# Performance work log

Hardware: AMD Instinct MI355X
Metric: run time of the kernel (lower is better)

The kernel has to match this reference:

```python
import jax, jax.numpy as jnp
import numpy as np

TEMPERATURE = 1.0
WEIGHT = 1.0


def _transitivity_sum(rel):
    """rel: [N, N] relation probabilities for one (batch, relation) slice.
    Computes sum_{a,b,c} relu(rel[a,b] - rel[a,c] * rel[b,c]) via a scan over c
    (outer product of column c), keeping memory at O(N^2) instead of O(N^3)."""
    def step(acc, col):  # col = rel[:, c], shape [N]
        viol = jax.nn.relu(rel - col[:, None] * col[None, :])  # [N, N]
        return acc + jnp.sum(viol), None
    acc, _ = jax.lax.scan(step, jnp.zeros((), rel.dtype), rel.T)
    return acc


def setup_inputs() -> dict:
    key = jax.random.key(0)
    B, N, R = 2, 512, 4
    relation_logits = jax.random.normal(key, (B, N, N, R), dtype=jnp.float32)
    entity_masks = jnp.ones((B, N), dtype=jnp.int32)
    return {"relation_logits": relation_logits, "entity_masks": entity_masks}


def reference(relation_logits, entity_masks):
    B, N, _, R = relation_logits.shape
    probs = jax.nn.sigmoid(relation_logits / TEMPERATURE)  # [B, N, N, R]
    m = (entity_masks > 0).astype(probs.dtype)             # [B, N]
    rel = probs * m[:, :, None, None] * m[:, None, :, None]
    # flatten (batch, relation) and vmap the per-matrix cubic reduction
    rel_br = jnp.transpose(rel, (0, 3, 1, 2)).reshape(B * R, N, N)
    per = jax.vmap(_transitivity_sum)(rel_br)              # [B*R]
    # per-batch loss = sum_r / R; final = weight * mean over batch
    return WEIGHT * jnp.sum(per) / (R * B)
```

## Files before the change

kernel.cpp:

```cpp
#include <hip/hip_runtime.h>
#include <math.h>

#define N      512
#define RNUM   4
#define BNUM   2
#define NSLICE (RNUM * BNUM)
#define TILE   128
#define CT     32
#define LSTR   136
#define CSPLIT 16
#define NCOLB  16
#define SCALE  0.0625f

typedef _Float16 half2_t __attribute__((ext_vector_type(2)));

__device__ __forceinline__ unsigned int h2u(half2_t h) {
  return __builtin_bit_cast(unsigned int, h);
}
__device__ __forceinline__ half2_t u2h(unsigned int u) {
  return __builtin_bit_cast(half2_t, u);
}

#if __has_builtin(__builtin_amdgcn_fdot2)
__device__ __forceinline__ float fdot2_(half2_t a, half2_t b, float c) {
  return __builtin_amdgcn_fdot2(a, b, c, false);
}
#else
__device__ __forceinline__ float fdot2_(half2_t a, half2_t b, float c) {
  return c + (float)a.x * (float)b.x + (float)a.y * (float)b.y;
}
#endif

__device__ __forceinline__ unsigned pk_fnma_bl(unsigned a, unsigned b, unsigned c) {
  unsigned d;
  asm("v_pk_fma_f16 %0, %1, %2, %3 op_sel:[0,0,0] op_sel_hi:[0,1,1] neg_lo:[1,0,0] neg_hi:[1,0,0]"
      : "=v"(d) : "v"(a), "v"(b), "v"(c));
  return d;
}
__device__ __forceinline__ unsigned pk_fnma_bh(unsigned a, unsigned b, unsigned c) {
  unsigned d;
  asm("v_pk_fma_f16 %0, %1, %2, %3 op_sel:[1,0,0] op_sel_hi:[1,1,1] neg_lo:[1,0,0] neg_hi:[1,0,0]"
      : "=v"(d) : "v"(a), "v"(b), "v"(c));
  return d;
}

__device__ __forceinline__ float sigmoidf_(float x) {
  return 1.0f / (1.0f + __expf(-x));
}

__device__ __forceinline__ unsigned packh2(float a, float b) {
  half2_t h = {(_Float16)a, (_Float16)b};
  return h2u(h);
}

__global__ void zero_out_kernel(float* out) { out[0] = 0.0f; }

__global__ __launch_bounds__(256) void prep_f16_kernel(const float* __restrict__ logits,
                                                       const int* __restrict__ masks,
                                                       _Float16* __restrict__ P,
                                                       float* __restrict__ out) {
  if (blockIdx.x == 0 && threadIdx.x == 0) out[0] = 0.0f;
  int t = blockIdx.x * 256 + threadIdx.x;
  int b = t >> 16;
  int rem4 = t & (N * N / 4 - 1);
  int i = rem4 >> 7;
  int j4 = rem4 & 127;
  const float4* Lp = ((const float4*)logits) + ((size_t)(b * N + i) * N + 4 * j4);
  float4 l0 = Lp[0], l1 = Lp[1], l2 = Lp[2], l3 = Lp[3];
  int4 mj = *(const int4*)(masks + b * N + 4 * j4);
  float mi = (masks[b * N + i] > 0) ? 1.0f : 0.0f;
  float m0 = mi * ((mj.x > 0) ? 1.0f : 0.0f);
  float m1 = mi * ((mj.y > 0) ? 1.0f : 0.0f);
  float m2 = mi * ((mj.z > 0) ? 1.0f : 0.0f);
  float m3 = mi * ((mj.w > 0) ? 1.0f : 0.0f);
  size_t off = (size_t)i * N + 4 * j4;
  _Float16* Pb = P + (size_t)b * RNUM * N * N + off;
  {
    uint2 v = {packh2(m0 * sigmoidf_(l0.x), m1 * sigmoidf_(l1.x)),
               packh2(m2 * sigmoidf_(l2.x), m3 * sigmoidf_(l3.x))};
    *(uint2*)(Pb + 0 * (size_t)N * N) = v;
  }
  {
    uint2 v = {packh2(m0 * sigmoidf_(l0.y), m1 * sigmoidf_(l1.y)),
               packh2(m2 * sigmoidf_(l2.y), m3 * sigmoidf_(l3.y))};
    *(uint2*)(Pb + 1 * (size_t)N * N) = v;
  }
  {
    uint2 v = {packh2(m0 * sigmoidf_(l0.z), m1 * sigmoidf_(l1.z)),
               packh2(m2 * sigmoidf_(l2.z), m3 * sigmoidf_(l3.z))};
    *(uint2*)(Pb + 2 * (size_t)N * N) = v;
  }
  {
    uint2 v = {packh2(m0 * sigmoidf_(l0.w), m1 * sigmoidf_(l1.w)),
               packh2(m2 * sigmoidf_(l2.w), m3 * sigmoidf_(l3.w))};
    *(uint2*)(Pb + 3 * (size_t)N * N) = v;
  }
}

__global__ __launch_bounds__(256, 4) void work_f16_kernel(const _Float16* __restrict__ P,
                                                          float* __restrict__ out) {
  __shared__ __align__(16) _Float16 tA[CT][LSTR];
  __shared__ __align__(16) _Float16 tB[CT][LSTR];
  __shared__ float wsum[4];

  const int tid = threadIdx.x;
  const int bid = blockIdx.x;

  if (bid < NCOLB) {
    const int s    = bid >> 1;
    const int half = bid & 1;
    const int c    = half * 256 + tid;
    const _Float16* col = P + (size_t)s * N * N + c;
    float sum = 0.0f;
#pragma unroll 16
    for (int a = 0; a < N; ++a) sum += (float)col[(size_t)a * N];
    float v = sum * ((float)N - sum);
    for (int off = 32; off > 0; off >>= 1) v += __shfl_down(v, off, 64);
    const int wid = tid >> 6;
    if ((tid & 63) == 0) wsum[wid] = v;
    __syncthreads();
    if (tid == 0)
      atomicAdd(out, (wsum[0] + wsum[1] + wsum[2] + wsum[3]) * SCALE);
    return;
  }

  const int m  = bid - NCOLB;
  const int bt = m & 3;
  const int at = (m >> 2) & 3;
  const int s  = (m >> 4) & 7;
  const int cz = m >> 7;
  const int a0 = at * TILE;
  const int b0 = bt * TILE;
  const int c0 = cz * CT;

  const int ta = tid & 15;
  const int tb = tid >> 4;

  const _Float16* Ph = P + (size_t)s * N * N;

  {
    const int u   = tid & 127;
    const int h   = tid >> 7;
    const int isB = u >> 6;
    const int p   = u & 63;
    const int r0  = (isB ? b0 : a0) + 2 * p;
    const int cc0 = c0 + h * 16;
    const _Float16* s0row = Ph + (size_t)r0 * N + cc0;
    const _Float16* s1row = s0row + N;
    _Float16* dst = isB ? &tB[h * 16][2 * p] : &tA[h * 16][2 * p];
    uint4 q0 = ((const uint4*)s0row)[0];
    uint4 q1 = ((const uint4*)s0row)[1];
    uint4 r0v = ((const uint4*)s1row)[0];
    uint4 r1v = ((const uint4*)s1row)[1];
    unsigned int w0[8] = {q0.x, q0.y, q0.z, q0.w, q1.x, q1.y, q1.z, q1.w};
    unsigned int w1[8] = {r0v.x, r0v.y, r0v.z, r0v.w, r1v.x, r1v.y, r1v.z, r1v.w};
#pragma unroll
    for (int k = 0; k < 8; ++k) {
      unsigned int lo = (w1[k] << 16) | (w0[k] & 0xFFFFu);
      unsigned int hi = (w1[k] & 0xFFFF0000u) | (w0[k] >> 16);
      *(unsigned int*)(dst + (size_t)(2 * k) * LSTR)     = lo;
      *(unsigned int*)(dst + (size_t)(2 * k + 1) * LSTR) = hi;
    }
  }

  unsigned rabw[8][4];
#pragma unroll
  for (int x = 0; x < 8; ++x) {
    int ga = a0 + ta * 8 + x;
    uint4 q = *(const uint4*)(Ph + (size_t)ga * N + b0 + tb * 8);
    rabw[x][0] = q.x; rabw[x][1] = q.y; rabw[x][2] = q.z; rabw[x][3] = q.w;
  }

  float acc[8];
  unsigned q16[8];
#pragma unroll
  for (int x = 0; x < 8; ++x) { acc[x] = 0.0f; q16[x] = 0u; }

  const half2_t kOne = {(_Float16)1.0f, (_Float16)1.0f};

  __syncthreads();

#pragma unroll 1
  for (int cg = 0; cg < CT / 4; ++cg) {
#pragma unroll
    for (int dc = 0; dc < 4; ++dc) {
      const int c = cg * 4 + dc;
      uint4 ua = *(const uint4*)&tA[c][ta * 8];
      uint4 ub = *(const uint4*)&tB[c][tb * 8];
      unsigned aw[4] = {ua.x, ua.y, ua.z, ua.w};
      unsigned bw[4] = {ub.x, ub.y, ub.z, ub.w};
#pragma unroll
      for (int k = 0; k < 4; ++k) {
#pragma unroll
        for (int yp = 0; yp < 4; ++yp) {
          unsigned tl = pk_fnma_bl(aw[k], bw[yp], rabw[2 * k][yp]);
          q16[2 * k] = h2u(u2h(q16[2 * k]) + u2h(tl & 0x7FFF7FFFu));
          unsigned th = pk_fnma_bh(aw[k], bw[yp], rabw[2 * k + 1][yp]);
          q16[2 * k + 1] = h2u(u2h(q16[2 * k + 1]) + u2h(th & 0x7FFF7FFFu));
        }
      }
    }
#pragma unroll
    for (int x = 0; x < 8; ++x) {
      acc[x] = fdot2_(u2h(q16[x]), kOne, acc[x]);
      q16[x] = 0u;
    }
  }

  float tsum = 0.0f;
#pragma unroll
  for (int x = 0; x < 8; ++x) tsum += acc[x];

  for (int off = 32; off > 0; off >>= 1) tsum += __shfl_down(tsum, off, 64);

  const int wid = tid >> 6;
  if ((tid & 63) == 0) wsum[wid] = tsum;
  __syncthreads();
  if (tid == 0)
    atomicAdd(out, (wsum[0] + wsum[1] + wsum[2] + wsum[3]) * SCALE);
}

#define FCT    64
#define FSTR   132
#define FCSPL  4

__global__ __launch_bounds__(256, 2) void work_f32_fallback(const float* __restrict__ logits,
                                                            const int* __restrict__ masks,
                                                            float* __restrict__ out) {
  __shared__ __align__(16) float tA[FCT][FSTR];
  __shared__ __align__(16) float tB[FCT][FSTR];
  __shared__ float wsum[4];

  const int tid = threadIdx.x;
  const int bid = blockIdx.x;

  if (bid < NCOLB) {
    const int s    = bid >> 1;
    const int half = bid & 1;
    const int c    = half * 256 + tid;
    const int bb   = s >> 2;
    const int r    = s & 3;
    const int* mrow = masks + bb * N;
    float mc = (mrow[c] > 0) ? 1.0f : 0.0f;
    float sum = 0.0f;
#pragma unroll 4
    for (int a = 0; a < N; ++a) {
      float ma = (mrow[a] > 0) ? 1.0f : 0.0f;
      size_t idx = ((size_t)(bb * N + a) * N + c) * RNUM + r;
      sum += sigmoidf_(logits[idx]) * ma * mc;
    }
    float v = sum * ((float)N - sum);
    for (int off = 32; off > 0; off >>= 1) v += __shfl_down(v, off, 64);
    const int wid = tid >> 6;
    if ((tid & 63) == 0) wsum[wid] = v;
    __syncthreads();
    if (tid == 0)
      atomicAdd(out, (wsum[0] + wsum[1] + wsum[2] + wsum[3]) * SCALE);
    return;
  }

  const int m  = bid - NCOLB;
  const int bt = m & 3;
  const int at = (m >> 2) & 3;
  const int s  = (m >> 4) & 7;
  const int cz = m >> 7;
  const int a0 = at * TILE;
  const int b0 = bt * TILE;
  const int bb = s >> 2;
  const int r  = s & 3;
  const int cbeg = cz * (N / FCSPL);
  const int cend = cbeg + (N / FCSPL);

  const int ta = tid & 15;
  const int tb = tid >> 4;
  const int* mrow = masks + bb * N;

  float rab[8][8];
#pragma unroll
  for (int x = 0; x < 8; ++x) {
    int ra = a0 + ((x >> 2) << 6) + ta * 4 + (x & 3);
    float ma = (mrow[ra] > 0) ? 1.0f : 0.0f;
#pragma unroll
    for (int y = 0; y < 8; ++y) {
      int cb = b0 + ((y >> 2) << 6) + tb * 4 + (y & 3);
      float mb = (mrow[cb] > 0) ? 1.0f : 0.0f;
      size_t idx = ((size_t)(bb * N + ra) * N + cb) * RNUM + r;
      rab[x][y] = sigmoidf_(logits[idx]) * ma * mb;
    }
  }

  float acc[8][2];
#pragma unroll
  for (int x = 0; x < 8; ++x) { acc[x][0] = 0.0f; acc[x][1] = 0.0f; }

  for (int c0 = cbeg; c0 < cend; c0 += FCT) {
    __syncthreads();
#pragma unroll
    for (int it = 0; it < 32; ++it) {
      int e = it * 256 + tid;
      int c = e & 63;
      int i = e >> 6;
      int pc = ((((i >> 2) ^ ((c >> 2) & 31)) & 31) << 2) | (i & 3);
      float mc = (mrow[c0 + c] > 0) ? 1.0f : 0.0f;
      {
        float mi = (mrow[a0 + i] > 0) ? 1.0f : 0.0f;
        size_t idx = ((size_t)(bb * N + a0 + i) * N + (c0 + c)) * RNUM + r;
        tA[c][pc] = sigmoidf_(logits[idx]) * mi * mc;
      }
      {
        float mi = (mrow[b0 + i] > 0) ? 1.0f : 0.0f;
        size_t idx = ((size_t)(bb * N + b0 + i) * N + (c0 + c)) * RNUM + r;
        tB[c][pc] = sigmoidf_(logits[idx]) * mi * mc;
      }
    }
    __syncthreads();

#pragma unroll 2
    for (int cg = 0; cg < FCT / 4; ++cg) {
      const float* pa = &tA[cg * 4][((ta ^ cg) & 31) << 2];
      const float* pb = &tB[cg * 4][((tb ^ cg) & 31) << 2];
#pragma unroll
      for (int dc = 0; dc < 4; ++dc) {
        float4 a0v = *(const float4*)(pa + dc * FSTR);
        float4 a1v = *(const float4*)(pa + dc * FSTR + 64);
        float4 b0v = *(const float4*)(pb + dc * FSTR);
        float4 b1v = *(const float4*)(pb + dc * FSTR + 64);
        float avv[8] = {a0v.x, a0v.y, a0v.z, a0v.w, a1v.x, a1v.y, a1v.z, a1v.w};
        float bvv[8] = {b0v.x, b0v.y, b0v.z, b0v.w, b1v.x, b1v.y, b1v.z, b1v.w};
#pragma unroll
        for (int x = 0; x < 8; ++x) {
#pragma unroll
          for (int y = 0; y < 4; ++y)
            acc[x][0] += fabsf(fmaf(-avv[x], bvv[y], rab[x][y]));
#pragma unroll
          for (int y = 4; y < 8; ++y)
            acc[x][1] += fabsf(fmaf(-avv[x], bvv[y], rab[x][y]));
        }
      }
    }
  }

  float tsum = 0.0f;
#pragma unroll
  for (int x = 0; x < 8; ++x) tsum += acc[x][0] + acc[x][1];
  for (int off = 32; off > 0; off >>= 1) tsum += __shfl_down(tsum, off, 64);
  const int wid = tid >> 6;
  if ((tid & 63) == 0) wsum[wid] = tsum;
  __syncthreads();
  if (tid == 0)
    atomicAdd(out, (wsum[0] + wsum[1] + wsum[2] + wsum[3]) * SCALE);
}

extern "C" void kernel_launch(void* const* d_in, const int* in_sizes, int n_in,
                              void* d_out, int out_size, void* d_ws, size_t ws_size,
                              hipStream_t stream) {
  const float* logits = (const float*)d_in[0];
  const int*   masks  = (const int*)d_in[1];
  float*       out    = (float*)d_out;

  const size_t P_BYTES = (size_t)NSLICE * N * N * sizeof(_Float16);

  if (ws_size >= P_BYTES) {
    _Float16* P = (_Float16*)d_ws;
    prep_f16_kernel<<<(BNUM * N * N / 4) / 256, 256, 0, stream>>>(logits, masks, P, out);
    const int nblocks = NCOLB + 4 * 4 * NSLICE * CSPLIT;
    work_f16_kernel<<<nblocks, 256, 0, stream>>>(P, out);
  } else {
    zero_out_kernel<<<1, 1, 0, stream>>>(out);
    const int nblocks = NCOLB + 4 * 4 * NSLICE * FCSPL;
    work_f32_fallback<<<nblocks, 256, 0, stream>>>(logits, masks, out);
  }
}
```

Baseline: 115.2 us.

## Replace packed-f16 inner loop with f32 FMA and abs on 512-thread blocks

The main tile kernel now turns the fp16 staged tiles into fp32 in shared memory and computes |r_ab - r_ac*r_bc| with scalar fp32 fmaf and fabsf. This replaces the packed v_pk_fma_f16 path that used two-level fp16/fp32 accumulation. Blocks grow to 512 threads, with each thread covering 8x4 outputs instead of 8x8, and the column-sum blocks are cut to one per slice. The aim is better precision and more occupancy, at the cost of half the packed arithmetic throughput and twice the shared-memory footprint.

```diff
diff --git a/kernel.cpp b/kernel.cpp
--- a/kernel.cpp
+++ b/kernel.cpp
@@ -7,50 +7,24 @@
 #define NSLICE (RNUM * BNUM)
 #define TILE   128
 #define CT     32
-#define LSTR   136
+#define LSTRF  132
 #define CSPLIT 16
-#define NCOLB  16
+#define NCOLB  8
 #define SCALE  0.0625f
 
 typedef _Float16 half2_t __attribute__((ext_vector_type(2)));
 
-__device__ __forceinline__ unsigned int h2u(half2_t h) {
-  return __builtin_bit_cast(unsigned int, h);
-}
 __device__ __forceinline__ half2_t u2h(unsigned int u) {
   return __builtin_bit_cast(half2_t, u);
 }
 
-#if __has_builtin(__builtin_amdgcn_fdot2)
-__device__ __forceinline__ float fdot2_(half2_t a, half2_t b, float c) {
-  return __builtin_amdgcn_fdot2(a, b, c, false);
-}
-#else
-__device__ __forceinline__ float fdot2_(half2_t a, half2_t b, float c) {
-  return c + (float)a.x * (float)b.x + (float)a.y * (float)b.y;
-}
-#endif
-
-__device__ __forceinline__ unsigned pk_fnma_bl(unsigned a, unsigned b, unsigned c) {
-  unsigned d;
-  asm("v_pk_fma_f16 %0, %1, %2, %3 op_sel:[0,0,0] op_sel_hi:[0,1,1] neg_lo:[1,0,0] neg_hi:[1,0,0]"
-      : "=v"(d) : "v"(a), "v"(b), "v"(c));
-  return d;
-}
-__device__ __forceinline__ unsigned pk_fnma_bh(unsigned a, unsigned b, unsigned c) {
-  unsigned d;
-  asm("v_pk_fma_f16 %0, %1, %2, %3 op_sel:[1,0,0] op_sel_hi:[1,1,1] neg_lo:[1,0,0] neg_hi:[1,0,0]"
-      : "=v"(d) : "v"(a), "v"(b), "v"(c));
-  return d;
-}
-
 __device__ __forceinline__ float sigmoidf_(float x) {
   return 1.0f / (1.0f + __expf(-x));
 }
 
 __device__ __forceinline__ unsigned packh2(float a, float b) {
   half2_t h = {(_Float16)a, (_Float16)b};
-  return h2u(h);
+  return __builtin_bit_cast(unsigned, h);
 }
 
 __global__ void zero_out_kernel(float* out) { out[0] = 0.0f; }
@@ -97,19 +71,18 @@
   }
 }
 
-__global__ __launch_bounds__(256, 4) void work_f16_kernel(const _Float16* __restrict__ P,
+__global__ __launch_bounds__(512, 8) void work_f16_kernel(const _Float16* __restrict__ P,
                                                           float* __restrict__ out) {
-  __shared__ __align__(16) _Float16 tA[CT][LSTR];
-  __shared__ __align__(16) _Float16 tB[CT][LSTR];
-  __shared__ float wsum[4];
+  __shared__ __align__(16) float tA[CT][LSTRF];
+  __shared__ __align__(16) float tB[CT][LSTRF];
+  __shared__ float wsum[8];
 
   const int tid = threadIdx.x;
   const int bid = blockIdx.x;
 
   if (bid < NCOLB) {
-    const int s    = bid >> 1;
-    const int half = bid & 1;
-    const int c    = half * 256 + tid;
+    const int s = bid;
+    const int c = tid;
     const _Float16* col = P + (size_t)s * N * N + c;
     float sum = 0.0f;
 #pragma unroll 16
@@ -119,8 +92,12 @@
     const int wid = tid >> 6;
     if ((tid & 63) == 0) wsum[wid] = v;
     __syncthreads();
-    if (tid == 0)
-      atomicAdd(out, (wsum[0] + wsum[1] + wsum[2] + wsum[3]) * SCALE);
+    if (tid == 0) {
+      float t = 0.0f;
+#pragma unroll
+      for (int w = 0; w < 8; ++w) t += wsum[w];
+      atomicAdd(out, t * SCALE);
+    }
     return;
   }
 
@@ -133,77 +110,63 @@
   const int b0 = bt * TILE;
   const int c0 = cz * CT;
 
-  const int ta = tid & 15;
-  const int tb = tid >> 4;
+  const int ta  = tid & 15;
+  const int tbg = tid >> 5;
+
+  const int tbgq = tid >> 4;
+  (void)tbg;
 
   const _Float16* Ph = P + (size_t)s * N * N;
 
   {
-    const int u   = tid & 127;
-    const int h   = tid >> 7;
-    const int isB = u >> 6;
-    const int p   = u & 63;
-    const int r0  = (isB ? b0 : a0) + 2 * p;
-    const int cc0 = c0 + h * 16;
-    const _Float16* s0row = Ph + (size_t)r0 * N + cc0;
-    const _Float16* s1row = s0row + N;
-    _Float16* dst = isB ? &tB[h * 16][2 * p] : &tA[h * 16][2 * p];
-    uint4 q0 = ((const uint4*)s0row)[0];
-    uint4 q1 = ((const uint4*)s0row)[1];
-    uint4 r0v = ((const uint4*)s1row)[0];
-    uint4 r1v = ((const uint4*)s1row)[1];
-    unsigned int w0[8] = {q0.x, q0.y, q0.z, q0.w, q1.x, q1.y, q1.z, q1.w};
-    unsigned int w1[8] = {r0v.x, r0v.y, r0v.z, r0v.w, r1v.x, r1v.y, r1v.z, r1v.w};
-#pragma unroll
-    for (int k = 0; k < 8; ++k) {
-      unsigned int lo = (w1[k] << 16) | (w0[k] & 0xFFFFu);
-      unsigned int hi = (w1[k] & 0xFFFF0000u) | (w0[k] >> 16);
-      *(unsigned int*)(dst + (size_t)(2 * k) * LSTR)     = lo;
-      *(unsigned int*)(dst + (size_t)(2 * k + 1) * LSTR) = hi;
-    }
-  }
-
-  unsigned rabw[8][4];
+    const int r   = tid & 127;
+    const int oct = tid >> 7;
+    const _Float16* sa = Ph + (size_t)(a0 + r) * N + c0 + oct * 8;
+    const _Float16* sb = Ph + (size_t)(b0 + r) * N + c0 + oct * 8;
+    uint4 qa = *(const uint4*)sa;
+    uint4 qb = *(const uint4*)sb;
+    unsigned wa[4] = {qa.x, qa.y, qa.z, qa.w};
+    unsigned wb[4] = {qb.x, qb.y, qb.z, qb.w};
+#pragma unroll
+    for (int k = 0; k < 4; ++k) {
+      half2_t ha = u2h(wa[k]);
+      half2_t hb = u2h(wb[k]);
+      tA[oct * 8 + 2 * k    ][r] = (float)ha.x;
+      tA[oct * 8 + 2 * k + 1][r] = (float)ha.y;
+      tB[oct * 8 + 2 * k    ][r] = (float)hb.x;
+      tB[oct * 8 + 2 * k + 1][r] = (float)hb.y;
+    }
+  }
+
+  float rabf[8][4];
 #pragma unroll
   for (int x = 0; x < 8; ++x) {
     int ga = a0 + ta * 8 + x;
-    uint4 q = *(const uint4*)(Ph + (size_t)ga * N + b0 + tb * 8);
-    rabw[x][0] = q.x; rabw[x][1] = q.y; rabw[x][2] = q.z; rabw[x][3] = q.w;
+    uint2 q = *(const uint2*)(Ph + (size_t)ga * N + b0 + tbgq * 4);
+    half2_t h0 = u2h(q.x);
+    half2_t h1 = u2h(q.y);
+    rabf[x][0] = (float)h0.x; rabf[x][1] = (float)h0.y;
+    rabf[x][2] = (float)h1.x; rabf[x][3] = (float)h1.y;
   }
 
   float acc[8];
-  unsigned q16[8];
-#pragma unroll
-  for (int x = 0; x < 8; ++x) { acc[x] = 0.0f; q16[x] = 0u; }
-
-  const half2_t kOne = {(_Float16)1.0f, (_Float16)1.0f};
+#pragma unroll
+  for (int x = 0; x < 8; ++x) acc[x] = 0.0f;
 
   __syncthreads();
 
-#pragma unroll 1
-  for (int cg = 0; cg < CT / 4; ++cg) {
-#pragma unroll
-    for (int dc = 0; dc < 4; ++dc) {
-      const int c = cg * 4 + dc;
-      uint4 ua = *(const uint4*)&tA[c][ta * 8];
-      uint4 ub = *(const uint4*)&tB[c][tb * 8];
-      unsigned aw[4] = {ua.x, ua.y, ua.z, ua.w};
-      unsigned bw[4] = {ub.x, ub.y, ub.z, ub.w};
-#pragma unroll
-      for (int k = 0; k < 4; ++k) {
-#pragma unroll
-        for (int yp = 0; yp < 4; ++yp) {
-          unsigned tl = pk_fnma_bl(aw[k], bw[yp], rabw[2 * k][yp]);
-          q16[2 * k] = h2u(u2h(q16[2 * k]) + u2h(tl & 0x7FFF7FFFu));
-          unsigned th = pk_fnma_bh(aw[k], bw[yp], rabw[2 * k + 1][yp]);
-          q16[2 * k + 1] = h2u(u2h(q16[2 * k + 1]) + u2h(th & 0x7FFF7FFFu));
-        }
-      }
-    }
+#pragma unroll 2
+  for (int c = 0; c < CT; ++c) {
+    float4 a0v = *(const float4*)&tA[c][ta * 8];
+    float4 a1v = *(const float4*)&tA[c][ta * 8 + 4];
+    float4 b0v = *(const float4*)&tB[c][tbgq * 4];
+    float av[8] = {a0v.x, a0v.y, a0v.z, a0v.w, a1v.x, a1v.y, a1v.z, a1v.w};
+    float bv[4] = {b0v.x, b0v.y, b0v.z, b0v.w};
 #pragma unroll
     for (int x = 0; x < 8; ++x) {
-      acc[x] = fdot2_(u2h(q16[x]), kOne, acc[x]);
-      q16[x] = 0u;
+#pragma unroll
+      for (int y = 0; y < 4; ++y)
+        acc[x] += fabsf(fmaf(-av[x], bv[y], rabf[x][y]));
     }
   }
 
@@ -216,13 +179,18 @@
   const int wid = tid >> 6;
   if ((tid & 63) == 0) wsum[wid] = tsum;
   __syncthreads();
-  if (tid == 0)
-    atomicAdd(out, (wsum[0] + wsum[1] + wsum[2] + wsum[3]) * SCALE);
+  if (tid == 0) {
+    float t = 0.0f;
+#pragma unroll
+    for (int w = 0; w < 8; ++w) t += wsum[w];
+    atomicAdd(out, t * SCALE);
+  }
 }
 
 #define FCT    64
 #define FSTR   132
 #define FCSPL  4
+#define FNCOLB 16
 
 __global__ __launch_bounds__(256, 2) void work_f32_fallback(const float* __restrict__ logits,
                                                             const int* __restrict__ masks,
@@ -234,7 +202,7 @@
   const int tid = threadIdx.x;
   const int bid = blockIdx.x;
 
-  if (bid < NCOLB) {
+  if (bid < FNCOLB) {
     const int s    = bid >> 1;
     const int half = bid & 1;
     const int c    = half * 256 + tid;
@@ -259,7 +227,7 @@
     return;
   }
 
-  const int m  = bid - NCOLB;
+  const int m  = bid - FNCOLB;
   const int bt = m & 3;
   const int at = (m >> 2) & 3;
   const int s  = (m >> 4) & 7;
@@ -364,10 +332,10 @@
     _Float16* P = (_Float16*)d_ws;
     prep_f16_kernel<<<(BNUM * N * N / 4) / 256, 256, 0, stream>>>(logits, masks, P, out);
     const int nblocks = NCOLB + 4 * 4 * NSLICE * CSPLIT;
-    work_f16_kernel<<<nblocks, 256, 0, stream>>>(P, out);
+    work_f16_kernel<<<nblocks, 512, 0, stream>>>(P, out);
   } else {
     zero_out_kernel<<<1, 1, 0, stream>>>(out);
-    const int nblocks = NCOLB + 4 * 4 * NSLICE * FCSPL;
+    const int nblocks = FNCOLB + 4 * 4 * NSLICE * FCSPL;
     work_f32_fallback<<<nblocks, 256, 0, stream>>>(logits, masks, out);
   }
 }
```

Measured after the change: 127.8 us. 1.11x slower.

## Process two c-chunks per block and accumulate each product via fdot2 into f32

Applied to the files above, without the earlier changes.

Each block now stages two 32-column chunks of the c dimension into two shared buffers, halving the number of c-split blocks. The second chunk's global loads are issued before compute on the first chunk begins. The inner loop drops the inline-asm packed FNMA and the f16 partial accumulator: it computes rab - a*b in half2, takes the absolute value via a sign mask, and adds it straight into f32 with fdot2. This trades the cheaper f16 accumulation for one dot instruction per pair and raises launch_bounds occupancy to 8, which may cause register pressure or spills.

```diff
diff --git a/kernel.cpp b/kernel.cpp
--- a/kernel.cpp
+++ b/kernel.cpp
@@ -8,7 +8,7 @@
 #define TILE   128
 #define CT     32
 #define LSTR   136
-#define CSPLIT 16
+#define CSPLIT 8
 #define NCOLB  16
 #define SCALE  0.0625f
 
@@ -30,19 +30,6 @@
   return c + (float)a.x * (float)b.x + (float)a.y * (float)b.y;
 }
 #endif
-
-__device__ __forceinline__ unsigned pk_fnma_bl(unsigned a, unsigned b, unsigned c) {
-  unsigned d;
-  asm("v_pk_fma_f16 %0, %1, %2, %3 op_sel:[0,0,0] op_sel_hi:[0,1,1] neg_lo:[1,0,0] neg_hi:[1,0,0]"
-      : "=v"(d) : "v"(a), "v"(b), "v"(c));
-  return d;
-}
-__device__ __forceinline__ unsigned pk_fnma_bh(unsigned a, unsigned b, unsigned c) {
-  unsigned d;
-  asm("v_pk_fma_f16 %0, %1, %2, %3 op_sel:[1,0,0] op_sel_hi:[1,1,1] neg_lo:[1,0,0] neg_hi:[1,0,0]"
-      : "=v"(d) : "v"(a), "v"(b), "v"(c));
-  return d;
-}
 
 __device__ __forceinline__ float sigmoidf_(float x) {
   return 1.0f / (1.0f + __expf(-x));
@@ -97,10 +84,10 @@
   }
 }
 
-__global__ __launch_bounds__(256, 4) void work_f16_kernel(const _Float16* __restrict__ P,
+__global__ __launch_bounds__(256, 8) void work_f16_kernel(const _Float16* __restrict__ P,
                                                           float* __restrict__ out) {
-  __shared__ __align__(16) _Float16 tA[CT][LSTR];
-  __shared__ __align__(16) _Float16 tB[CT][LSTR];
+  __shared__ __align__(16) _Float16 tA[2][CT][LSTR];
+  __shared__ __align__(16) _Float16 tB[2][CT][LSTR];
   __shared__ float wsum[4];
 
   const int tid = threadIdx.x;
@@ -131,81 +118,87 @@
   const int cz = m >> 7;
   const int a0 = at * TILE;
   const int b0 = bt * TILE;
-  const int c0 = cz * CT;
+  const int c0 = cz * (2 * CT);
 
   const int ta = tid & 15;
   const int tb = tid >> 4;
 
   const _Float16* Ph = P + (size_t)s * N * N;
 
-  {
-    const int u   = tid & 127;
-    const int h   = tid >> 7;
-    const int isB = u >> 6;
-    const int p   = u & 63;
-    const int r0  = (isB ? b0 : a0) + 2 * p;
-    const int cc0 = c0 + h * 16;
-    const _Float16* s0row = Ph + (size_t)r0 * N + cc0;
-    const _Float16* s1row = s0row + N;
-    _Float16* dst = isB ? &tB[h * 16][2 * p] : &tA[h * 16][2 * p];
-    uint4 q0 = ((const uint4*)s0row)[0];
-    uint4 q1 = ((const uint4*)s0row)[1];
-    uint4 r0v = ((const uint4*)s1row)[0];
-    uint4 r1v = ((const uint4*)s1row)[1];
-    unsigned int w0[8] = {q0.x, q0.y, q0.z, q0.w, q1.x, q1.y, q1.z, q1.w};
-    unsigned int w1[8] = {r0v.x, r0v.y, r0v.z, r0v.w, r1v.x, r1v.y, r1v.z, r1v.w};
-#pragma unroll
-    for (int k = 0; k < 8; ++k) {
-      unsigned int lo = (w1[k] << 16) | (w0[k] & 0xFFFFu);
-      unsigned int hi = (w1[k] & 0xFFFF0000u) | (w0[k] >> 16);
-      *(unsigned int*)(dst + (size_t)(2 * k) * LSTR)     = lo;
-      *(unsigned int*)(dst + (size_t)(2 * k + 1) * LSTR) = hi;
-    }
-  }
-
-  unsigned rabw[8][4];
+  const int su   = tid & 127;
+  const int sh   = tid >> 7;
+  const int sisB = su >> 6;
+  const int sp   = su & 63;
+  const int srow = (sisB ? b0 : a0) + 2 * sp;
+
+#define STAGE_CHUNK(cc, buf)                                                   \
+  {                                                                            \
+    const _Float16* s0row = Ph + (size_t)srow * N + (cc) + sh * 16;            \
+    const _Float16* s1row = s0row + N;                                         \
+    _Float16* dst = sisB ? &tB[buf][sh * 16][2 * sp] : &tA[buf][sh * 16][2 * sp]; \
+    uint4 q0 = ((const uint4*)s0row)[0];                                       \
+    uint4 q1 = ((const uint4*)s0row)[1];                                       \
+    uint4 r0v = ((const uint4*)s1row)[0];                                      \
+    uint4 r1v = ((const uint4*)s1row)[1];                                      \
+    unsigned int w0[8] = {q0.x, q0.y, q0.z, q0.w, q1.x, q1.y, q1.z, q1.w};     \
+    unsigned int w1[8] = {r0v.x, r0v.y, r0v.z, r0v.w, r1v.x, r1v.y, r1v.z, r1v.w}; \
+    _Pragma("unroll")                                                          \
+    for (int k = 0; k < 8; ++k) {                                              \
+      unsigned int lo = (w1[k] << 16) | (w0[k] & 0xFFFFu);                     \
+      unsigned int hi = (w1[k] & 0xFFFF0000u) | (w0[k] >> 16);                 \
+      *(unsigned int*)(dst + (size_t)(2 * k) * LSTR)     = lo;                 \
+      *(unsigned int*)(dst + (size_t)(2 * k + 1) * LSTR) = hi;                 \
+    }                                                                          \
+  }
+
+  STAGE_CHUNK(c0, 0)
+
+  half2_t rab2[8][4];
 #pragma unroll
   for (int x = 0; x < 8; ++x) {
     int ga = a0 + ta * 8 + x;
     uint4 q = *(const uint4*)(Ph + (size_t)ga * N + b0 + tb * 8);
-    rabw[x][0] = q.x; rabw[x][1] = q.y; rabw[x][2] = q.z; rabw[x][3] = q.w;
+    rab2[x][0] = u2h(q.x); rab2[x][1] = u2h(q.y);
+    rab2[x][2] = u2h(q.z); rab2[x][3] = u2h(q.w);
   }
 
   float acc[8];
-  unsigned q16[8];
-#pragma unroll
-  for (int x = 0; x < 8; ++x) { acc[x] = 0.0f; q16[x] = 0u; }
+#pragma unroll
+  for (int x = 0; x < 8; ++x) acc[x] = 0.0f;
 
   const half2_t kOne = {(_Float16)1.0f, (_Float16)1.0f};
 
   __syncthreads();
 
-#pragma unroll 1
-  for (int cg = 0; cg < CT / 4; ++cg) {
-#pragma unroll
-    for (int dc = 0; dc < 4; ++dc) {
-      const int c = cg * 4 + dc;
-      uint4 ua = *(const uint4*)&tA[c][ta * 8];
-      uint4 ub = *(const uint4*)&tB[c][tb * 8];
-      unsigned aw[4] = {ua.x, ua.y, ua.z, ua.w};
-      unsigned bw[4] = {ub.x, ub.y, ub.z, ub.w};
-#pragma unroll
-      for (int k = 0; k < 4; ++k) {
-#pragma unroll
-        for (int yp = 0; yp < 4; ++yp) {
-          unsigned tl = pk_fnma_bl(aw[k], bw[yp], rabw[2 * k][yp]);
-          q16[2 * k] = h2u(u2h(q16[2 * k]) + u2h(tl & 0x7FFF7FFFu));
-          unsigned th = pk_fnma_bh(aw[k], bw[yp], rabw[2 * k + 1][yp]);
-          q16[2 * k + 1] = h2u(u2h(q16[2 * k + 1]) + u2h(th & 0x7FFF7FFFu));
-        }
-      }
-    }
-#pragma unroll
-    for (int x = 0; x < 8; ++x) {
-      acc[x] = fdot2_(u2h(q16[x]), kOne, acc[x]);
-      q16[x] = 0u;
-    }
-  }
+  STAGE_CHUNK(c0 + CT, 1)
+
+#define COMPUTE_CHUNK(buf)                                                     \
+  _Pragma("unroll 4")                                                          \
+  for (int c = 0; c < CT; ++c) {                                               \
+    uint4 ua = *(const uint4*)&tA[buf][c][ta * 8];                             \
+    uint4 ub = *(const uint4*)&tB[buf][c][tb * 8];                             \
+    half2_t av[4] = {u2h(ua.x), u2h(ua.y), u2h(ua.z), u2h(ua.w)};              \
+    half2_t bv[4] = {u2h(ub.x), u2h(ub.y), u2h(ub.z), u2h(ub.w)};              \
+    _Pragma("unroll")                                                          \
+    for (int x = 0; x < 8; ++x) {                                              \
+      _Float16 as = (x & 1) ? av[x >> 1].y : av[x >> 1].x;                     \
+      half2_t asp = {as, as};                                                  \
+      float a_ = acc[x];                                                       \
+      _Pragma("unroll")                                                        \
+      for (int yp = 0; yp < 4; ++yp) {                                         \
+        half2_t t2 = rab2[x][yp] - asp * bv[yp];       \
+        half2_t p2 = u2h(h2u(t2) & 0x7FFF7FFFu);               \
+        a_ = fdot2_(p2, kOne, a_);                         \
+      }                                                                        \
+      acc[x] = a_;                                                             \
+    }                                                                          \
+  }
+
+  COMPUTE_CHUNK(0)
+
+  __syncthreads();
+
+  COMPUTE_CHUNK(1)
 
   float tsum = 0.0f;
 #pragma unroll
@@ -218,11 +211,15 @@
   __syncthreads();
   if (tid == 0)
     atomicAdd(out, (wsum[0] + wsum[1] + wsum[2] + wsum[3]) * SCALE);
+
+#undef STAGE_CHUNK
+#undef COMPUTE_CHUNK
 }
 
 #define FCT    64
 #define FSTR   132
 #define FCSPL  4
+#define FNCOLB 16
 
 __global__ __launch_bounds__(256, 2) void work_f32_fallback(const float* __restrict__ logits,
                                                             const int* __restrict__ masks,
@@ -234,7 +231,7 @@
   const int tid = threadIdx.x;
   const int bid = blockIdx.x;
 
-  if (bid < NCOLB) {
+  if (bid < FNCOLB) {
     const int s    = bid >> 1;
     const int half = bid & 1;
     const int c    = half * 256 + tid;
@@ -259,7 +256,7 @@
     return;
   }
 
-  const int m  = bid - NCOLB;
+  const int m  = bid - FNCOLB;
   const int bt = m & 3;
   const int at = (m >> 2) & 3;
   const int s  = (m >> 4) & 7;
@@ -367,7 +364,7 @@
     work_f16_kernel<<<nblocks, 256, 0, stream>>>(P, out);
   } else {
     zero_out_kernel<<<1, 1, 0, stream>>>(out);
-    const int nblocks = NCOLB + 4 * 4 * NSLICE * FCSPL;
+    const int nblocks = FNCOLB + 4 * 4 * NSLICE * FCSPL;
     work_f32_fallback<<<nblocks, 256, 0, stream>>>(logits, masks, out);
   }
 }
```

Measured after the change: 115.0 us. No clear change (-0.2%).
